# Optimization experiments

Hardware: AMD Instinct MI355X
Metric: run time of the kernel (lower is better)

## Reference

```python
import jax, jax.numpy as jnp
import numpy as np

H = W = 128          # feature-map height/width
WS = 8               # window size
SHIFT = 4            # cyclic shift (ws // 2)
HEADS = 3
C = 96               # hidden size (head_dim = 32)
MLP_FACTOR = 4
N = WS * WS          # tokens per window
NW = (H // WS) * (W // WS)  # windows per image


def _rel_pos_index():
    coords = np.stack(np.meshgrid(np.arange(WS), np.arange(WS), indexing='ij')).reshape(2, -1)
    rel = (coords[:, :, None] - coords[:, None, :]).transpose(1, 2, 0)
    rel[:, :, 0] += WS - 1
    rel[:, :, 1] += WS - 1
    rel[:, :, 0] *= 2 * WS - 1
    return rel.sum(-1)  # (N, N) int


def _window_partition_np(img):  # (H, W) -> (NW, N)
    x = img.reshape(H // WS, WS, W // WS, WS)
    return x.transpose(0, 2, 1, 3).reshape(-1, N)


def _attn_mask():
    img = np.zeros((H, W))
    cnt = 0
    sl = (slice(0, -WS), slice(-WS, -SHIFT), slice(-SHIFT, None))
    for hs in sl:
        for ws_ in sl:
            img[hs, ws_] = cnt
            cnt += 1
    win = _window_partition_np(img)
    return np.where(win[:, None, :] != win[:, :, None], -100.0, 0.0).astype(np.float32)


REL_IDX = jnp.asarray(_rel_pos_index().reshape(-1))   # (N*N,)
ATTN_MASK = jnp.asarray(_attn_mask())                 # (NW, N, N)


def _layernorm(x, g, b, eps=1e-5):
    m = x.mean(-1, keepdims=True)
    v = ((x - m) ** 2).mean(-1, keepdims=True)
    return (x - m) * jax.lax.rsqrt(v + eps) * g + b


def setup_inputs() -> dict:
    key = jax.random.key(0)
    ks = jax.random.split(key, 8)
    B = 16
    s = 0.02  # random_normal_initializer(0.0, 0.02)
    return {
        'x': jax.random.normal(ks[0], (B, H * W, C), jnp.float32),
        'ln1_g': jnp.ones((C,), jnp.float32),
        'ln1_b': jnp.zeros((C,), jnp.float32),
        'qkv_w': jax.random.normal(ks[1], (C, 3 * C), jnp.float32) * s,
        'qkv_b': jnp.zeros((3 * C,), jnp.float32),
        'proj_w': jax.random.normal(ks[2], (C, C), jnp.float32) * s,
        'bias_table': jax.random.normal(ks[3], ((2 * WS - 1) ** 2, HEADS), jnp.float32) * s,
        'ln2_g': jnp.ones((C,), jnp.float32),
        'ln2_b': jnp.zeros((C,), jnp.float32),
        'mlp_w1': jax.random.normal(ks[4], (C, MLP_FACTOR * C), jnp.float32) * s,
        'mlp_w2': jax.random.normal(ks[5], (MLP_FACTOR * C, C), jnp.float32) * s,
    }


def reference(x, ln1_g, ln1_b, qkv_w, qkv_b, proj_w, bias_table, ln2_g, ln2_b, mlp_w1, mlp_w2):
    B = x.shape[0]
    shortcut = x
    h = _layernorm(x, ln1_g, ln1_b).reshape(B, H, W, C)
    # cyclic shift
    h = jnp.roll(h, (-SHIFT, -SHIFT), axis=(1, 2))
    # window partition: (B*NW, N, C)
    h = h.reshape(B, H // WS, WS, W // WS, WS, C).transpose(0, 1, 3, 2, 4, 5).reshape(B * NW, N, C)
    # windowed MHSA
    qkv = h @ qkv_w + qkv_b
    qkv = qkv.reshape(B * NW, N, 3, HEADS, C // HEADS).transpose(2, 0, 3, 1, 4)
    q, k, v = qkv[0], qkv[1], qkv[2]
    scale = (C // HEADS) ** -0.5
    attn = jnp.einsum('whnd,whmd->whnm', q * scale, k)
    bias = bias_table[REL_IDX].reshape(N, N, HEADS).transpose(2, 0, 1)
    attn = attn + bias[None]
    attn = attn.reshape(B, NW, HEADS, N, N) + ATTN_MASK[None, :, None]
    attn = jax.nn.softmax(attn, axis=-1).reshape(B * NW, HEADS, N, N)
    out = jnp.einsum('whnm,whmd->whnd', attn, v).transpose(0, 2, 1, 3).reshape(B * NW, N, C)
    out = out @ proj_w
    # window reverse + un-shift
    out = out.reshape(B, H // WS, W // WS, WS, WS, C).transpose(0, 1, 3, 2, 4, 5).reshape(B, H, W, C)
    out = jnp.roll(out, (SHIFT, SHIFT), axis=(1, 2)).reshape(B, H * W, C)
    x = shortcut + out
    # MLP branch
    h2 = _layernorm(x, ln2_g, ln2_b)
    h2 = jax.nn.gelu(h2 @ mlp_w1) @ mlp_w2
    return x + h2
```

## Files before the change

### kernel.cpp

```cpp
#include <hip/hip_runtime.h>

#define SHIFT 4

typedef __bf16 bf16x8 __attribute__((ext_vector_type(8)));
typedef __bf16 bf16x4 __attribute__((ext_vector_type(4)));
typedef float  f32x4  __attribute__((ext_vector_type(4)));

#define LDA 104
#define LDV 72
#define LDU 72
#define LDW1 104
#define LDW2 72

#define WS_W1T  36864
#define WS_W2C  73728
#define WS_BIAS_BYTES 221184

__global__ __launch_bounds__(256)
void swin_prep_kernel(const float* __restrict__ qkvw, const float* __restrict__ projw,
                      const float* __restrict__ w1, const float* __restrict__ w2,
                      const float* __restrict__ btab,
                      __bf16* __restrict__ ws)
{
  const int i = blockIdx.x * 256 + threadIdx.x;
  if (i < 36864) {
    const int fi = i >> 9, e = i & 511;
    const int lane = e >> 3, j = e & 7;
    const int l15 = lane & 15;
    const int kk  = (lane >> 4) * 8 + j;
    float v;
    if (fi < 54) {
      const int c = fi / 18, rem = fi % 18, t = rem / 3, ks = rem % 3;
      v = qkvw[(ks * 32 + kk) * 288 + c * 96 + t * 16 + l15];
    } else {
      const int f2 = fi - 54, t = f2 / 3, ks = f2 % 3;
      v = projw[(ks * 32 + kk) * 96 + t * 16 + l15];
    }
    ws[i] = (__bf16)v;
  } else if (i < 73728) {
    const int j = i - WS_W1T;
    const int col = j / 96, kk = j - col * 96;
    ws[i] = (__bf16)w1[kk * 384 + col];
  } else if (i < 110592) {
    const int j = i - WS_W2C;
    const int cc = j / 6144, r2 = j - cc * 6144;
    const int o = r2 / 64, jl = r2 - o * 64;
    ws[i] = (__bf16)w2[(cc * 64 + jl) * 96 + o];
  } else {
    const int jj = i - 110592;
    const int h = jj >> 12, n = (jj >> 6) & 63, m = jj & 63;
    const int dy = (n >> 3) - (m >> 3), dx = (n & 7) - (m & 7);
    float* biasf = (float*)((char*)ws + WS_BIAS_BYTES);
    biasf[jj] = btab[((dy + 7) * 15 + (dx + 7)) * 3 + h];
  }
}

__global__ __launch_bounds__(256, 4)
void swin_block_kernel(const float* __restrict__ x,
                       const float* __restrict__ ln1g, const float* __restrict__ ln1b,
                       const __bf16* __restrict__ ws, const float* __restrict__ qkvb,
                       const float* __restrict__ ln2g, const float* __restrict__ ln2b,
                       float* __restrict__ out)
{
  __shared__ __align__(16) char lds[40448];
  __bf16* h_s = (__bf16*)lds;
  __bf16* k_s = (__bf16*)(lds + 13312);
  __bf16* v_s = (__bf16*)(lds + 26624);
  __bf16* u_s = (__bf16*)(lds + 13312);
  __bf16* w_s = (__bf16*)(lds + 26624);

  const float* biasf = (const float*)((const char*)ws + WS_BIAS_BYTES);

  const int tid  = threadIdx.x;
  const int lane = tid & 63;
  const int wv   = tid >> 6;
  const int l15  = lane & 15;
  const int g4   = lane >> 4;
  const int blk  = blockIdx.x;
  const int b    = blk >> 8;
  const int wy   = (blk >> 4) & 15;
  const int wx   = blk & 15;

  {
    const int t = tid >> 2, p = tid & 3;
    const int ti = t >> 3, tj = t & 7;
    const int iy = (wy * 8 + ti + SHIFT) & 127;
    const int ix = (wx * 8 + tj + SHIFT) & 127;
    const float* rowp = x + ((size_t)(b * 16384 + iy * 128 + ix)) * 96 + p * 24;
    float vb[24];
    float s = 0.f, ss = 0.f;
#pragma unroll
    for (int u = 0; u < 6; ++u) {
      f32x4 f = *(const f32x4*)(rowp + 4 * u);
#pragma unroll
      for (int e = 0; e < 4; ++e) { float q = f[e]; vb[4*u+e] = q; s += q; ss += q*q; }
    }
    s  += __shfl_xor(s, 1);  s  += __shfl_xor(s, 2);
    ss += __shfl_xor(ss, 1); ss += __shfl_xor(ss, 2);
    const float mean = s * (1.f / 96.f);
    const float var  = ss * (1.f / 96.f) - mean * mean;
    const float rstd = rsqrtf(var + 1e-5f);
#pragma unroll
    for (int u = 0; u < 6; ++u) {
      f32x4 gg = *(const f32x4*)(ln1g + p * 24 + 4 * u);
      f32x4 bb = *(const f32x4*)(ln1b + p * 24 + 4 * u);
      f32x4 nv;
#pragma unroll
      for (int e = 0; e < 4; ++e) nv[e] = (vb[4*u+e] - mean) * rstd * gg[e] + bb[e];
      *(bf16x4*)&h_s[t * LDA + p * 24 + 4 * u] = __builtin_convertvector(nv, bf16x4);
    }
  }

  const float qscale = 0.17677669529663687f;
  const __bf16* fbase = ws + (size_t)lane * 8;
  const int rowb = 16 * wv;
  bf16x8 aq3[3];
#pragma unroll
  for (int c = 0; c < 3; ++c) {
    bf16x8 wf[6][3];
#pragma unroll
    for (int t = 0; t < 6; ++t)
#pragma unroll
      for (int ks = 0; ks < 3; ++ks)
        wf[t][ks] = *(const bf16x8*)(fbase + (size_t)(c * 18 + t * 3 + ks) * 512);
    f32x4 acc[6];
#pragma unroll
    for (int t = 0; t < 6; ++t) {
      const float bv = qkvb[c * 96 + t * 16 + l15];
      f32x4 a4 = {bv, bv, bv, bv};
      acc[t] = a4;
    }
#pragma unroll
    for (int ks = 0; ks < 3; ++ks) {
      bf16x8 a = *(const bf16x8*)&h_s[(rowb + l15) * LDA + ks * 32 + 8 * g4];
#pragma unroll
      for (int t = 0; t < 6; ++t)
        acc[t] = __builtin_amdgcn_mfma_f32_16x16x32_bf16(a, wf[t][ks], acc[t], 0, 0, 0);
    }
    if (c == 0) {
#pragma unroll
      for (int t = 0; t < 6; ++t) {
        const int col = (t >> 1) * 32 + (t & 1) * 16 + l15;
#pragma unroll
        for (int r = 0; r < 4; ++r)
          k_s[(rowb + 4 * g4 + r) * LDA + col] = (__bf16)(acc[t][r] * qscale);
      }
#pragma unroll
      for (int h = 0; h < 3; ++h)
        aq3[h] = *(const bf16x8*)&k_s[(rowb + l15) * LDA + h * 32 + 8 * g4];
    } else if (c == 1) {
#pragma unroll
      for (int t = 0; t < 6; ++t) {
        const int col = (t >> 1) * 32 + (t & 1) * 16 + l15;
#pragma unroll
        for (int r = 0; r < 4; ++r)
          k_s[(rowb + 4 * g4 + r) * LDA + col] = (__bf16)acc[t][r];
      }
    } else {
#pragma unroll
      for (int t = 0; t < 6; ++t) {
        const int head = t >> 1, dim = (t & 1) * 16 + l15;
        *(bf16x4*)&v_s[(head * 32 + dim) * LDV + rowb + 4 * g4] =
            __builtin_convertvector(acc[t], bf16x4);
      }
    }
  }

  __syncthreads();

  int qry[4], qrx[4];
#pragma unroll
  for (int r = 0; r < 4; ++r) {
    const int row = rowb + 4 * g4 + r;
    const int ti2 = row >> 3, tj2 = row & 7;
    qry[r] = (wy == 15) ? (ti2 < 4 ? 1 : 2) : 0;
    qrx[r] = (wx == 15) ? (tj2 < 4 ? 1 : 2) : 0;
  }
  const f32x4 zf = {0.f, 0.f, 0.f, 0.f};
  f32x4 ovA[3][2];
#pragma unroll
  for (int h = 0; h < 3; ++h) {
    const float* bh = biasf + h * 4096;
    float bv[4][4];
#pragma unroll
    for (int n = 0; n < 4; ++n)
#pragma unroll
      for (int r = 0; r < 4; ++r)
        bv[n][r] = bh[(rowb + 4 * g4 + r) * 64 + n * 16 + l15];

    f32x4 sc[4];
#pragma unroll
    for (int n = 0; n < 4; ++n) {
      bf16x8 bk = *(const bf16x8*)&k_s[(n * 16 + l15) * LDA + h * 32 + 8 * g4];
      sc[n] = __builtin_amdgcn_mfma_f32_16x16x32_bf16(aq3[h], bk, zf, 0, 0, 0);
    }
#pragma unroll
    for (int n = 0; n < 4; ++n) {
      const int colt = n * 16 + l15;
      const int ki = colt >> 3, kj = colt & 7;
      const int kry = (wy == 15) ? (ki < 4 ? 1 : 2) : 0;
      const int krx = (wx == 15) ? (kj < 4 ? 1 : 2) : 0;
#pragma unroll
      for (int r = 0; r < 4; ++r) {
        const float mk = (qry[r] == kry && qrx[r] == krx) ? 0.f : -100.f;
        sc[n][r] += bv[n][r] + mk;
      }
    }
    float mx[4], sm[4];
#pragma unroll
    for (int r = 0; r < 4; ++r) {
      float m = fmaxf(fmaxf(sc[0][r], sc[1][r]), fmaxf(sc[2][r], sc[3][r]));
      m = fmaxf(m, __shfl_xor(m, 1)); m = fmaxf(m, __shfl_xor(m, 2));
      m = fmaxf(m, __shfl_xor(m, 4)); m = fmaxf(m, __shfl_xor(m, 8));
      mx[r] = m; sm[r] = 0.f;
    }
#pragma unroll
    for (int n = 0; n < 4; ++n)
#pragma unroll
      for (int r = 0; r < 4; ++r) {
        float p = __expf(sc[n][r] - mx[r]); sc[n][r] = p; sm[r] += p;
      }
#pragma unroll
    for (int r = 0; r < 4; ++r) {
      float s2 = sm[r];
      s2 += __shfl_xor(s2, 1); s2 += __shfl_xor(s2, 2);
      s2 += __shfl_xor(s2, 4); s2 += __shfl_xor(s2, 8);
      sm[r] = __builtin_amdgcn_rcpf(s2);
    }
#pragma unroll
    for (int n = 0; n < 4; ++n)
#pragma unroll
      for (int r = 0; r < 4; ++r)
        h_s[(rowb + 4 * g4 + r) * LDA + n * 16 + l15] = (__bf16)sc[n][r];
    f32x4 ov[2] = {zf, zf};
#pragma unroll
    for (int ks = 0; ks < 2; ++ks) {
      bf16x8 pa = *(const bf16x8*)&h_s[(rowb + l15) * LDA + ks * 32 + 8 * g4];
#pragma unroll
      for (int t2 = 0; t2 < 2; ++t2) {
        bf16x8 vb2 = *(const bf16x8*)&v_s[(h * 32 + t2 * 16 + l15) * LDV + ks * 32 + 8 * g4];
        ov[t2] = __builtin_amdgcn_mfma_f32_16x16x32_bf16(pa, vb2, ov[t2], 0, 0, 0);
      }
    }
#pragma unroll
    for (int t2 = 0; t2 < 2; ++t2)
#pragma unroll
      for (int r = 0; r < 4; ++r)
        ovA[h][t2][r] = ov[t2][r] * sm[r];
  }
#pragma unroll
  for (int h = 0; h < 3; ++h)
#pragma unroll
    for (int t2 = 0; t2 < 2; ++t2)
#pragma unroll
      for (int r = 0; r < 4; ++r)
        h_s[(rowb + 4 * g4 + r) * LDA + h * 32 + t2 * 16 + l15] = (__bf16)ovA[h][t2][r];

  f32x4 po[6];
#pragma unroll
  for (int t = 0; t < 6; ++t) po[t] = zf;
#pragma unroll
  for (int ks = 0; ks < 3; ++ks) {
    bf16x8 a = *(const bf16x8*)&h_s[(rowb + l15) * LDA + ks * 32 + 8 * g4];
#pragma unroll
    for (int t = 0; t < 6; ++t) {
      bf16x8 bb = *(const bf16x8*)(fbase + (size_t)(54 + t * 3 + ks) * 512);
      po[t] = __builtin_amdgcn_mfma_f32_16x16x32_bf16(a, bb, po[t], 0, 0, 0);
    }
  }

  size_t gbase[4];
  float xm[6][4];
#pragma unroll
  for (int r = 0; r < 4; ++r) {
    const int row = rowb + 4 * g4 + r;
    const int ti2 = row >> 3, tj2 = row & 7;
    const int iy = (wy * 8 + ti2 + SHIFT) & 127;
    const int ix = (wx * 8 + tj2 + SHIFT) & 127;
    gbase[r] = ((size_t)(b * 16384 + iy * 128 + ix)) * 96;
#pragma unroll
    for (int t = 0; t < 6; ++t)
      xm[t][r] = x[gbase[r] + t * 16 + l15] + po[t][r];
  }
  {
    float g6[6], b6[6];
#pragma unroll
    for (int t = 0; t < 6; ++t) { g6[t] = ln2g[t * 16 + l15]; b6[t] = ln2b[t * 16 + l15]; }
#pragma unroll
    for (int r = 0; r < 4; ++r) {
      float s = 0.f, ss = 0.f;
#pragma unroll
      for (int t = 0; t < 6; ++t) { s += xm[t][r]; ss += xm[t][r] * xm[t][r]; }
      s  += __shfl_xor(s, 1);  s  += __shfl_xor(s, 2);
      s  += __shfl_xor(s, 4);  s  += __shfl_xor(s, 8);
      ss += __shfl_xor(ss, 1); ss += __shfl_xor(ss, 2);
      ss += __shfl_xor(ss, 4); ss += __shfl_xor(ss, 8);
      const float mean = s * (1.f / 96.f);
      const float var  = ss * (1.f / 96.f) - mean * mean;
      const float rstd = rsqrtf(var + 1e-5f);
#pragma unroll
      for (int t = 0; t < 6; ++t) {
        const float h2 = (xm[t][r] - mean) * rstd * g6[t] + b6[t];
        h_s[(rowb + 4 * g4 + r) * LDA + t * 16 + l15] = (__bf16)h2;
      }
    }
  }

  __syncthreads();

  f32x4 acc[6];
#pragma unroll
  for (int t = 0; t < 6; ++t) acc[t] = zf;

  for (int cc = 0; cc < 6; ++cc) {
    {
      const __bf16* wsrc = ws + WS_W1T + cc * 6144;
#pragma unroll
      for (int m = tid; m < 768; m += 256) {
        const int row = m / 12, q4 = m - row * 12;
        *(uint4*)&w_s[row * LDW1 + q4 * 8] = *(const uint4*)&wsrc[row * 96 + q4 * 8];
      }
    }
    __syncthreads();
    f32x4 ua[4];
#pragma unroll
    for (int t = 0; t < 4; ++t) ua[t] = zf;
#pragma unroll
    for (int ks = 0; ks < 3; ++ks) {
      bf16x8 a = *(const bf16x8*)&h_s[(rowb + l15) * LDA + ks * 32 + 8 * g4];
#pragma unroll
      for (int t = 0; t < 4; ++t) {
        bf16x8 bb = *(const bf16x8*)&w_s[(t * 16 + l15) * LDW1 + ks * 32 + 8 * g4];
        ua[t] = __builtin_amdgcn_mfma_f32_16x16x32_bf16(a, bb, ua[t], 0, 0, 0);
      }
    }
#pragma unroll
    for (int t = 0; t < 4; ++t)
#pragma unroll
      for (int r = 0; r < 4; ++r) {
        const float v = ua[t][r];
        const float e = __expf(1.5957691216057308f * (v + 0.044715f * v * v * v));
        const float g = v - v * __builtin_amdgcn_rcpf(e + 1.f);
        u_s[(rowb + 4 * g4 + r) * LDU + t * 16 + l15] = (__bf16)g;
      }
    __syncthreads();
    {
      const __bf16* wsrc = ws + WS_W2C + cc * 6144;
#pragma unroll
      for (int m = tid; m < 768; m += 256) {
        const int row = m >> 3, q4 = m & 7;
        *(uint4*)&w_s[row * LDW2 + q4 * 8] = *(const uint4*)&wsrc[row * 64 + q4 * 8];
      }
    }
    __syncthreads();
#pragma unroll
    for (int ks = 0; ks < 2; ++ks) {
      bf16x8 pa = *(const bf16x8*)&u_s[(rowb + l15) * LDU + ks * 32 + 8 * g4];
#pragma unroll
      for (int t = 0; t < 6; ++t) {
        bf16x8 bb = *(const bf16x8*)&w_s[(t * 16 + l15) * LDW2 + ks * 32 + 8 * g4];
        acc[t] = __builtin_amdgcn_mfma_f32_16x16x32_bf16(pa, bb, acc[t], 0, 0, 0);
      }
    }
    __syncthreads();
  }

#pragma unroll
  for (int r = 0; r < 4; ++r)
#pragma unroll
    for (int t = 0; t < 6; ++t)
      out[gbase[r] + t * 16 + l15] = xm[t][r] + acc[t][r];
}

extern "C" void kernel_launch(void* const* d_in, const int* in_sizes, int n_in,
                              void* d_out, int out_size, void* d_ws, size_t ws_size,
                              hipStream_t stream) {
  (void)in_sizes; (void)n_in; (void)out_size; (void)ws_size;
  const float* x     = (const float*)d_in[0];
  const float* ln1g  = (const float*)d_in[1];
  const float* ln1b  = (const float*)d_in[2];
  const float* qkvw  = (const float*)d_in[3];
  const float* qkvb  = (const float*)d_in[4];
  const float* projw = (const float*)d_in[5];
  const float* btab  = (const float*)d_in[6];
  const float* ln2g  = (const float*)d_in[7];
  const float* ln2b  = (const float*)d_in[8];
  const float* w1    = (const float*)d_in[9];
  const float* w2    = (const float*)d_in[10];
  float* out = (float*)d_out;
  __bf16* ws = (__bf16*)d_ws;

  swin_prep_kernel<<<480, 256, 0, stream>>>(qkvw, projw, w1, w2, btab, ws);
  swin_block_kernel<<<4096, 256, 0, stream>>>(x, ln1g, ln1b, ws, qkvb, ln2g, ln2b, out);
}
```

Baseline: 166.6 us.

## Register-prefetch MLP weight chunks, raise MFMA priority, remap blocks across XCDs

MLP weight chunks are now prefetched into registers one iteration ahead, so the global load latency overlaps compute instead of stalling before each LDS store. MFMA loops are wrapped in s_setprio so matrix work gets issue priority over other waves. The block index is remapped so consecutive blocks spread across the 8 XCDs, with neighbouring windows sharing an XCD's L2. In exchange, register pressure rises by 6 uint4 per thread and a wasted wrap-around prefetch occurs on the last iteration.

```diff
diff --git a/kernel.cpp b/kernel.cpp
--- a/kernel.cpp
+++ b/kernel.cpp
@@ -76,10 +76,19 @@
   const int wv   = tid >> 6;
   const int l15  = lane & 15;
   const int g4   = lane >> 4;
-  const int blk  = blockIdx.x;
+  const int bid  = blockIdx.x;
+  const int blk  = (bid & 7) * 512 + (bid >> 3);
   const int b    = blk >> 8;
   const int wy   = (blk >> 4) & 15;
   const int wx   = blk & 15;
+
+  uint4 w1r[3], w2r[3];
+  {
+    const uint4* s1 = (const uint4*)(ws + WS_W1T);
+    const uint4* s2 = (const uint4*)(ws + WS_W2C);
+#pragma unroll
+    for (int q = 0; q < 3; ++q) { w1r[q] = s1[tid + q * 256]; w2r[q] = s2[tid + q * 256]; }
+  }
 
   {
     const int t = tid >> 2, p = tid & 3;
@@ -130,6 +139,7 @@
       f32x4 a4 = {bv, bv, bv, bv};
       acc[t] = a4;
     }
+    __builtin_amdgcn_s_setprio(1);
 #pragma unroll
     for (int ks = 0; ks < 3; ++ks) {
       bf16x8 a = *(const bf16x8*)&h_s[(rowb + l15) * LDA + ks * 32 + 8 * g4];
@@ -137,6 +147,7 @@
       for (int t = 0; t < 6; ++t)
         acc[t] = __builtin_amdgcn_mfma_f32_16x16x32_bf16(a, wf[t][ks], acc[t], 0, 0, 0);
     }
+    __builtin_amdgcn_s_setprio(0);
     if (c == 0) {
 #pragma unroll
       for (int t = 0; t < 6; ++t) {
@@ -189,11 +200,13 @@
         bv[n][r] = bh[(rowb + 4 * g4 + r) * 64 + n * 16 + l15];
 
     f32x4 sc[4];
+    __builtin_amdgcn_s_setprio(1);
 #pragma unroll
     for (int n = 0; n < 4; ++n) {
       bf16x8 bk = *(const bf16x8*)&k_s[(n * 16 + l15) * LDA + h * 32 + 8 * g4];
       sc[n] = __builtin_amdgcn_mfma_f32_16x16x32_bf16(aq3[h], bk, zf, 0, 0, 0);
     }
+    __builtin_amdgcn_s_setprio(0);
 #pragma unroll
     for (int n = 0; n < 4; ++n) {
       const int colt = n * 16 + l15;
@@ -233,6 +246,7 @@
       for (int r = 0; r < 4; ++r)
         h_s[(rowb + 4 * g4 + r) * LDA + n * 16 + l15] = (__bf16)sc[n][r];
     f32x4 ov[2] = {zf, zf};
+    __builtin_amdgcn_s_setprio(1);
 #pragma unroll
     for (int ks = 0; ks < 2; ++ks) {
       bf16x8 pa = *(const bf16x8*)&h_s[(rowb + l15) * LDA + ks * 32 + 8 * g4];
@@ -242,6 +256,7 @@
         ov[t2] = __builtin_amdgcn_mfma_f32_16x16x32_bf16(pa, vb2, ov[t2], 0, 0, 0);
       }
     }
+    __builtin_amdgcn_s_setprio(0);
 #pragma unroll
     for (int t2 = 0; t2 < 2; ++t2)
 #pragma unroll
@@ -259,6 +274,7 @@
   f32x4 po[6];
 #pragma unroll
   for (int t = 0; t < 6; ++t) po[t] = zf;
+  __builtin_amdgcn_s_setprio(1);
 #pragma unroll
   for (int ks = 0; ks < 3; ++ks) {
     bf16x8 a = *(const bf16x8*)&h_s[(rowb + l15) * LDA + ks * 32 + 8 * g4];
@@ -268,6 +284,7 @@
       po[t] = __builtin_amdgcn_mfma_f32_16x16x32_bf16(a, bb, po[t], 0, 0, 0);
     }
   }
+  __builtin_amdgcn_s_setprio(0);
 
   size_t gbase[4];
   float xm[6][4];
@@ -313,18 +330,22 @@
   for (int t = 0; t < 6; ++t) acc[t] = zf;
 
   for (int cc = 0; cc < 6; ++cc) {
+#pragma unroll
+    for (int q = 0; q < 3; ++q) {
+      const int m = tid + q * 256;
+      *(uint4*)&w_s[(m / 12) * LDW1 + (m % 12) * 8] = w1r[q];
+    }
     {
-      const __bf16* wsrc = ws + WS_W1T + cc * 6144;
-#pragma unroll
-      for (int m = tid; m < 768; m += 256) {
-        const int row = m / 12, q4 = m - row * 12;
-        *(uint4*)&w_s[row * LDW1 + q4 * 8] = *(const uint4*)&wsrc[row * 96 + q4 * 8];
-      }
+      const int nc = (cc == 5) ? 0 : cc + 1;
+      const uint4* s1 = (const uint4*)(ws + WS_W1T + nc * 6144);
+#pragma unroll
+      for (int q = 0; q < 3; ++q) w1r[q] = s1[tid + q * 256];
     }
     __syncthreads();
     f32x4 ua[4];
 #pragma unroll
     for (int t = 0; t < 4; ++t) ua[t] = zf;
+    __builtin_amdgcn_s_setprio(1);
 #pragma unroll
     for (int ks = 0; ks < 3; ++ks) {
       bf16x8 a = *(const bf16x8*)&h_s[(rowb + l15) * LDA + ks * 32 + 8 * g4];
@@ -334,6 +355,7 @@
         ua[t] = __builtin_amdgcn_mfma_f32_16x16x32_bf16(a, bb, ua[t], 0, 0, 0);
       }
     }
+    __builtin_amdgcn_s_setprio(0);
 #pragma unroll
     for (int t = 0; t < 4; ++t)
 #pragma unroll
@@ -344,15 +366,19 @@
         u_s[(rowb + 4 * g4 + r) * LDU + t * 16 + l15] = (__bf16)g;
       }
     __syncthreads();
+#pragma unroll
+    for (int q = 0; q < 3; ++q) {
+      const int m = tid + q * 256;
+      *(uint4*)&w_s[(m >> 3) * LDW2 + (m & 7) * 8] = w2r[q];
+    }
     {
-      const __bf16* wsrc = ws + WS_W2C + cc * 6144;
-#pragma unroll
-      for (int m = tid; m < 768; m += 256) {
-        const int row = m >> 3, q4 = m & 7;
-        *(uint4*)&w_s[row * LDW2 + q4 * 8] = *(const uint4*)&wsrc[row * 64 + q4 * 8];
-      }
+      const int nc = (cc == 5) ? 0 : cc + 1;
+      const uint4* s2 = (const uint4*)(ws + WS_W2C + nc * 6144);
+#pragma unroll
+      for (int q = 0; q < 3; ++q) w2r[q] = s2[tid + q * 256];
     }
     __syncthreads();
+    __builtin_amdgcn_s_setprio(1);
 #pragma unroll
     for (int ks = 0; ks < 2; ++ks) {
       bf16x8 pa = *(const bf16x8*)&u_s[(rowb + l15) * LDU + ks * 32 + 8 * g4];
@@ -362,6 +388,7 @@
         acc[t] = __builtin_amdgcn_mfma_f32_16x16x32_bf16(pa, bb, acc[t], 0, 0, 0);
       }
     }
+    __builtin_amdgcn_s_setprio(0);
     __syncthreads();
   }
 
```

Result: slower. 277.1 us (+66.3%).
